# Kernel optimization log

Measured on AMD Instinct MI355X. Metric: run time of the kernel, lower is better.

The kernel has to match this reference:

```python
import jax, jax.numpy as jnp
import numpy as np

LEVEL = 16            # number of spike time steps (q levels)
POS_MAX = float(LEVEL - 1)   # sym=False: pos_max = level-1
NEG_MIN = 0.0                # sym=False: neg_min = 0


def setup_inputs() -> dict:
    key = jax.random.key(0)
    x = jax.random.normal(key, (32, 2048, 1024), dtype=jnp.float32)
    return {"input": x}


def reference(input) -> jnp.ndarray:
    x = input
    ori_shape = x.shape
    N = x.shape[0]
    # [level, N//level, ...]
    xr = x.reshape((LEVEL, N // LEVEL) + x.shape[1:])
    # q_threshold init (module has init=True on first call); detached in original
    v_th = jax.lax.stop_gradient(
        jnp.abs(xr.sum(axis=0)).mean() * 2.0 / jnp.sqrt(POS_MAX)
    )
    # flatten(1): [Time, M]
    x_seq = xr.reshape(LEVEL, -1)

    v0 = jnp.zeros_like(x_seq[0]) + 0.5 * v_th
    T0 = jnp.zeros_like(x_seq[0])

    def step(carry, x_t):
        v, T = carry
        v = v + x_t
        pos = (v - v_th >= 0) & (T - POS_MAX < 0)
        neg = (v < 0) & (T - NEG_MIN > 0)
        # original assigns +1 first then -1 (neg overrides), so where(neg,...) outermost
        spike = jnp.where(neg, -1.0, jnp.where(pos, 1.0, 0.0)).astype(v.dtype)
        v = v - v_th * spike
        T = T + spike
        return (v, T), spike

    (_, _), spikes = jax.lax.scan(step, (v0, T0), x_seq)
    # output = spike_seq.reshape(ori_shape) * s_scale  (s_scale value == q_threshold)
    return spikes.reshape(ori_shape) * v_th
```

## Files before the change

kernel.cpp:

```cpp
#include <hip/hip_runtime.h>
#include <math.h>

#define LEVEL 16
#define RED_BLOCKS 2048
#define RED_THREADS 256

typedef float f32x4 __attribute__((ext_vector_type(4)));

__global__ __launch_bounds__(RED_THREADS) void colsum_abs_partial(
    const f32x4* __restrict__ x, double* __restrict__ partial, int M4)
{
    int tid = blockIdx.x * blockDim.x + threadIdx.x;
    int nthreads = gridDim.x * blockDim.x;

    double acc = 0.0;
    for (int m = tid; m < M4; m += nthreads) {
        float sx = 0.f, sy = 0.f, sz = 0.f, sw = 0.f;
        #pragma unroll
        for (int t = 0; t < LEVEL; ++t) {
            f32x4 v = x[(size_t)t * M4 + m];
            sx += v.x; sy += v.y; sz += v.z; sw += v.w;
        }
        acc += (double)fabsf(sx) + (double)fabsf(sy)
             + (double)fabsf(sz) + (double)fabsf(sw);
    }

    for (int off = 32; off > 0; off >>= 1)
        acc += __shfl_down(acc, off, 64);

    __shared__ double wsum[RED_THREADS / 64];
    int lane = threadIdx.x & 63;
    int wid  = threadIdx.x >> 6;
    if (lane == 0) wsum[wid] = acc;
    __syncthreads();
    if (threadIdx.x == 0) {
        double b = 0.0;
        #pragma unroll
        for (int w = 0; w < RED_THREADS / 64; ++w) b += wsum[w];
        partial[blockIdx.x] = b;
    }
}

__global__ __launch_bounds__(256) void finalize_vth(
    const double* __restrict__ partial, float* __restrict__ vth_out, int nb, int Mtotal)
{
    __shared__ double sdata[256];
    double a = 0.0;
    for (int i = threadIdx.x; i < nb; i += blockDim.x) a += partial[i];
    sdata[threadIdx.x] = a;
    __syncthreads();
    for (int s = 128; s > 0; s >>= 1) {
        if (threadIdx.x < s) sdata[threadIdx.x] += sdata[threadIdx.x + s];
        __syncthreads();
    }
    if (threadIdx.x == 0) {
        float mean = (float)(sdata[0] / (double)Mtotal);
        vth_out[0] = mean * 2.0f / sqrtf(15.0f);
    }
}

__global__ __launch_bounds__(256) void bif_scan(
    const f32x4* __restrict__ x, f32x4* __restrict__ out,
    const float* __restrict__ vth_p, int M4)
{
    int bid = gridDim.x - 1 - blockIdx.x;
    int m = bid * blockDim.x + threadIdx.x;
    if (m >= M4) return;

    const float vth = vth_p[0];

    f32x4 xv[LEVEL];
    #pragma unroll
    for (int t = 0; t < LEVEL; ++t)
        xv[t] = __builtin_nontemporal_load(&x[(size_t)t * M4 + m]);

    float v[4], T[4];
    #pragma unroll
    for (int c = 0; c < 4; ++c) { v[c] = 0.5f * vth; T[c] = 0.f; }

    #pragma unroll
    for (int t = 0; t < LEVEL; ++t) {
        float in[4] = { xv[t].x, xv[t].y, xv[t].z, xv[t].w };
        f32x4 ov;
        #pragma unroll
        for (int c = 0; c < 4; ++c) {
            float vv = v[c] + in[c];
            bool pos = ((vv - vth) >= 0.f) && ((T[c] - 15.f) < 0.f);
            bool neg = (vv < 0.f) && (T[c] > 0.f);
            float spike = neg ? -1.f : (pos ? 1.f : 0.f);
            vv -= vth * spike;
            T[c] += spike;
            v[c] = vv;
            ov[c] = spike * vth;
        }
        __builtin_nontemporal_store(ov, &out[(size_t)t * M4 + m]);
    }
}

extern "C" void kernel_launch(void* const* d_in, const int* in_sizes, int n_in,
                              void* d_out, int out_size, void* d_ws, size_t ws_size,
                              hipStream_t stream)
{
    const float* x = (const float*)d_in[0];
    float* out = (float*)d_out;
    const int total = in_sizes[0];
    const int M = total / LEVEL;
    const int M4 = M / 4;

    double* partials = (double*)d_ws;
    float* vth = (float*)((char*)d_ws + RED_BLOCKS * sizeof(double));

    colsum_abs_partial<<<RED_BLOCKS, RED_THREADS, 0, stream>>>(
        (const f32x4*)x, partials, M4);

    finalize_vth<<<1, 256, 0, stream>>>(partials, vth, RED_BLOCKS, M);

    int blocks = (M4 + 255) / 256;
    bif_scan<<<blocks, 256, 0, stream>>>(
        (const f32x4*)x, (f32x4*)out, vth, M4);
}
```

Baseline: 491.6 us.

## Fuse reduction, threshold, and scan into one cooperative kernel with grid sync

Replaces the three launches (partial abs-sum, finalize, scan) with a single cooperative kernel of 1024 blocks. It reduces partials, does a grid-wide sync, and has every block recompute the threshold redundantly before running a grid-stride BIF scan. This removes two launch gaps and the separate finalize kernel. In exchange it adds grid.sync cost, and the scan phase now runs with fewer resident blocks and grid-stride loops, which may hurt latency hiding. It falls back to the old path if the cooperative launch fails.

```diff
diff --git a/kernel.cpp b/kernel.cpp
--- a/kernel.cpp
+++ b/kernel.cpp
@@ -1,17 +1,26 @@
 #include <hip/hip_runtime.h>
+#include <hip/hip_cooperative_groups.h>
 #include <math.h>
 
 #define LEVEL 16
+#define COOP_BLOCKS 1024
+#define THREADS 256
+
 #define RED_BLOCKS 2048
 #define RED_THREADS 256
 
 typedef float f32x4 __attribute__((ext_vector_type(4)));
 
-__global__ __launch_bounds__(RED_THREADS) void colsum_abs_partial(
-    const f32x4* __restrict__ x, double* __restrict__ partial, int M4)
-{
-    int tid = blockIdx.x * blockDim.x + threadIdx.x;
-    int nthreads = gridDim.x * blockDim.x;
+namespace cg = cooperative_groups;
+
+__global__ __launch_bounds__(THREADS, 4) void bif_fused(
+    const f32x4* __restrict__ x, f32x4* __restrict__ out,
+    double* __restrict__ partial, int M4, int Mtotal)
+{
+    cg::grid_group grid = cg::this_grid();
+
+    const int tid = blockIdx.x * blockDim.x + threadIdx.x;
+    const int nthreads = gridDim.x * blockDim.x;
 
     double acc = 0.0;
     for (int m = tid; m < M4; m += nthreads) {
@@ -24,7 +33,90 @@
         acc += (double)fabsf(sx) + (double)fabsf(sy)
              + (double)fabsf(sz) + (double)fabsf(sw);
     }
-
+    for (int off = 32; off > 0; off >>= 1)
+        acc += __shfl_down(acc, off, 64);
+
+    __shared__ double wsum[THREADS / 64];
+    if ((threadIdx.x & 63) == 0) wsum[threadIdx.x >> 6] = acc;
+    __syncthreads();
+    if (threadIdx.x == 0) {
+        double b = 0.0;
+        #pragma unroll
+        for (int w = 0; w < THREADS / 64; ++w) b += wsum[w];
+        partial[blockIdx.x] = b;
+    }
+
+    grid.sync();
+
+    __shared__ double sred[THREADS];
+    {
+        const int per = COOP_BLOCKS / THREADS;
+        double s = 0.0;
+        #pragma unroll
+        for (int k = 0; k < per; ++k)
+            s += partial[threadIdx.x * per + k];
+        sred[threadIdx.x] = s;
+    }
+    __syncthreads();
+    for (int s = THREADS / 2; s > 0; s >>= 1) {
+        if (threadIdx.x < s) sred[threadIdx.x] += sred[threadIdx.x + s];
+        __syncthreads();
+    }
+    __shared__ float s_vth;
+    if (threadIdx.x == 0) {
+        float mean = (float)(sred[0] / (double)Mtotal);
+        s_vth = mean * 2.0f / sqrtf(15.0f);
+    }
+    __syncthreads();
+    const float vth = s_vth;
+
+    for (int m = tid; m < M4; m += nthreads) {
+        f32x4 xv[LEVEL];
+        #pragma unroll
+        for (int t = 0; t < LEVEL; ++t)
+            xv[t] = __builtin_nontemporal_load(&x[(size_t)t * M4 + m]);
+
+        float v[4], T[4];
+        #pragma unroll
+        for (int c = 0; c < 4; ++c) { v[c] = 0.5f * vth; T[c] = 0.f; }
+
+        #pragma unroll
+        for (int t = 0; t < LEVEL; ++t) {
+            float in[4] = { xv[t].x, xv[t].y, xv[t].z, xv[t].w };
+            f32x4 ov;
+            #pragma unroll
+            for (int c = 0; c < 4; ++c) {
+                float vv = v[c] + in[c];
+                bool pos = ((vv - vth) >= 0.f) && ((T[c] - 15.f) < 0.f);
+                bool neg = (vv < 0.f) && (T[c] > 0.f);
+                float spike = neg ? -1.f : (pos ? 1.f : 0.f);
+                vv -= vth * spike;
+                T[c] += spike;
+                v[c] = vv;
+                ov[c] = spike * vth;
+            }
+            __builtin_nontemporal_store(ov, &out[(size_t)t * M4 + m]);
+        }
+    }
+}
+
+__global__ __launch_bounds__(RED_THREADS) void colsum_abs_partial(
+    const f32x4* __restrict__ x, double* __restrict__ partial, int M4)
+{
+    int tid = blockIdx.x * blockDim.x + threadIdx.x;
+    int nthreads = gridDim.x * blockDim.x;
+
+    double acc = 0.0;
+    for (int m = tid; m < M4; m += nthreads) {
+        float sx = 0.f, sy = 0.f, sz = 0.f, sw = 0.f;
+        #pragma unroll
+        for (int t = 0; t < LEVEL; ++t) {
+            f32x4 v = x[(size_t)t * M4 + m];
+            sx += v.x; sy += v.y; sz += v.z; sw += v.w;
+        }
+        acc += (double)fabsf(sx) + (double)fabsf(sy)
+             + (double)fabsf(sz) + (double)fabsf(sw);
+    }
     for (int off = 32; off > 0; off >>= 1)
         acc += __shfl_down(acc, off, 64);
 
@@ -104,18 +196,28 @@
     const float* x = (const float*)d_in[0];
     float* out = (float*)d_out;
     const int total = in_sizes[0];
-    const int M = total / LEVEL;
-    const int M4 = M / 4;
+    int M = total / LEVEL;
+    int M4 = M / 4;
 
     double* partials = (double*)d_ws;
     float* vth = (float*)((char*)d_ws + RED_BLOCKS * sizeof(double));
 
-    colsum_abs_partial<<<RED_BLOCKS, RED_THREADS, 0, stream>>>(
-        (const f32x4*)x, partials, M4);
-
-    finalize_vth<<<1, 256, 0, stream>>>(partials, vth, RED_BLOCKS, M);
-
-    int blocks = (M4 + 255) / 256;
-    bif_scan<<<blocks, 256, 0, stream>>>(
-        (const f32x4*)x, (f32x4*)out, vth, M4);
-}
+    const f32x4* xv = (const f32x4*)x;
+    f32x4* outv = (f32x4*)out;
+
+    void* args[] = { (void*)&xv, (void*)&outv, (void*)&partials,
+                     (void*)&M4, (void*)&M };
+    hipError_t e = hipLaunchCooperativeKernel(
+        (const void*)bif_fused, dim3(COOP_BLOCKS), dim3(THREADS),
+        args, 0, stream);
+
+    if (e != hipSuccess) {
+        (void)hipGetLastError();
+        colsum_abs_partial<<<RED_BLOCKS, RED_THREADS, 0, stream>>>(
+            (const f32x4*)x, partials, M4);
+        finalize_vth<<<1, 256, 0, stream>>>(partials, vth, RED_BLOCKS, M);
+        int blocks = (M4 + 255) / 256;
+        bif_scan<<<blocks, 256, 0, stream>>>(
+            (const f32x4*)x, (f32x4*)outv, vth, M4);
+    }
+}
```

Result: slower. 547.8 us (+11.4%).
